# Optimization experiments

Hardware: AMD Instinct MI355X
Metric: run time of the kernel (lower is better)

Reference implementation:

```python
import jax, jax.numpy as jnp
import numpy as np

B, S, D, H = 1, 2048, 1024, 16
DH = D // H  # 64
HID = 4 * D
EPS = 1e-5
NEG = -1.0e9


def setup_inputs() -> dict:
    key = jax.random.key(0)
    ks = jax.random.split(key, 12)
    s = 0.02
    return {
        "y": jax.random.normal(ks[0], (B, S, D), jnp.float32),
        "encoder_output": jax.random.normal(ks[1], (B, S, D), jnp.float32),
        # per-head shared projection (query_fc used for q,k,v — faithful to source bug)
        "Wq_self": jax.random.normal(ks[2], (H, D, DH), jnp.float32) * s,
        "bq_self": jax.random.normal(ks[3], (H, DH), jnp.float32) * s,
        "Wq_cross": jax.random.normal(ks[4], (H, D, DH), jnp.float32) * s,
        "bq_cross": jax.random.normal(ks[5], (H, DH), jnp.float32) * s,
        "g1": jnp.ones((D,), jnp.float32), "beta1": jnp.zeros((D,), jnp.float32),
        "g2": jnp.ones((D,), jnp.float32), "beta2": jnp.zeros((D,), jnp.float32),
        "g3": jnp.ones((D,), jnp.float32), "beta3": jnp.zeros((D,), jnp.float32),
        "w1": jax.random.normal(ks[6], (D, HID), jnp.float32) * s,
        "b1": jax.random.normal(ks[7], (HID,), jnp.float32) * s,
        "w2": jax.random.normal(ks[8], (HID, D), jnp.float32) * s,
        "b2": jax.random.normal(ks[9], (D,), jnp.float32) * s,
    }


def _layernorm(x, g, b):
    mu = jnp.mean(x, axis=-1, keepdims=True)
    var = jnp.mean((x - mu) ** 2, axis=-1, keepdims=True)
    return (x - mu) * jax.lax.rsqrt(var + EPS) * g + b


def _mha(x_q, x_kv, W, bias, causal):
    # source bug: q, k, v all use query_fc projection
    q = jnp.einsum('bsd,hde->bhse', x_q, W) + bias[None, :, None, :]
    k = jnp.einsum('bsd,hde->bhse', x_kv, W) + bias[None, :, None, :]
    v = jnp.einsum('bsd,hde->bhse', x_kv, W) + bias[None, :, None, :]
    scores = jnp.einsum('bhse,bhte->bhst', q, k) / jnp.sqrt(jnp.float32(DH))
    if causal:
        sq, sk = scores.shape[-2], scores.shape[-1]
        mask = jnp.triu(jnp.ones((sq, sk), bool), k=1)
        scores = jnp.where(mask, NEG, scores)
    p = jax.nn.softmax(scores, axis=-1)
    out = jnp.einsum('bhst,bhte->bhse', p, v)  # [B,H,S,DH]
    b, h, s, e = out.shape
    return out.transpose(0, 2, 1, 3).reshape(b, s, h * e)


def reference(y, encoder_output, Wq_self, bq_self, Wq_cross, bq_cross,
              g1, beta1, g2, beta2, g3, beta3, w1, b1, w2, b2):
    sa = _mha(y, y, Wq_self, bq_self, causal=True)
    y1 = _layernorm(y + sa, g1, beta1)
    ca = _mha(y1, encoder_output, Wq_cross, bq_cross, causal=False)
    y2 = _layernorm(y1 + ca, g2, beta2)
    ff = jnp.maximum(y2 @ w1 + b1, 0.0) @ w2 + b2
    return _layernorm(y2 + ff, g3, beta3)
```

## Files before the change

kernel.cpp:

```cpp
#include <hip/hip_runtime.h>
#include <hip/hip_bf16.h>


#define S_LEN 2048
#define DMODEL 1024
#define NHEAD 16
#define DHEAD 64
#define HIDDEN 4096

using bf16 = __hip_bfloat16;
typedef __attribute__((ext_vector_type(8))) short bf16x8;
typedef __attribute__((ext_vector_type(4))) float floatx4;

__device__ __forceinline__ void async_ld16(const void* g, void* l) {
  __builtin_amdgcn_global_load_lds(
      (const __attribute__((address_space(1))) unsigned int*)g,
      (__attribute__((address_space(3))) unsigned int*)l, 16, 0, 0);
}

__device__ __forceinline__ unsigned short f2bf_bits(float f) {
  __hip_bfloat16 b = __float2bfloat16(f);
  return *(unsigned short*)&b;
}

template <bool HEADB>
__global__ __launch_bounds__(256) void transp_bf16_kernel(
    const float* __restrict__ src0, bf16* __restrict__ dst0,
    const float* __restrict__ src1, bf16* __restrict__ dst1, int K, int N) {
  const float* src = blockIdx.z ? src1 : src0;
  bf16* dst = blockIdx.z ? dst1 : dst0;
  __shared__ float tile[32][33];
  const int tx = threadIdx.x & 31, ty = threadIdx.x >> 5;
  const int k0 = blockIdx.y * 32, n0 = blockIdx.x * 32;
#pragma unroll
  for (int i = 0; i < 4; ++i) {
    const int k = k0 + ty + i * 8;
    const int n = n0 + tx;
    size_t idx;
    if (HEADB)
      idx = (size_t)(n >> 6) * ((size_t)K * 64) + (size_t)k * 64 + (n & 63);
    else
      idx = (size_t)k * N + n;
    tile[ty + i * 8][tx] = src[idx];
  }
  __syncthreads();
#pragma unroll
  for (int i = 0; i < 4; ++i) {
    const int n = n0 + ty + i * 8;
    const int k = k0 + tx;
    dst[(size_t)n * K + k] = __float2bfloat16(tile[tx][ty + i * 8]);
  }
}

__global__ __launch_bounds__(256) void conv_bf16_kernel(
    const float* __restrict__ src0, bf16* __restrict__ dst0,
    const float* __restrict__ src1, bf16* __restrict__ dst1, int n4) {
  const float* src = blockIdx.z ? src1 : src0;
  bf16* dst = blockIdx.z ? dst1 : dst0;
  const int i = blockIdx.x * 256 + threadIdx.x;
  if (i >= n4) return;
  float4 v = ((const float4*)src)[i];
  unsigned short r[4] = {f2bf_bits(v.x), f2bf_bits(v.y), f2bf_bits(v.z), f2bf_bits(v.w)};
  ((ushort2*)dst)[i * 2] = make_ushort2(r[0], r[1]);
  ((ushort2*)dst)[i * 2 + 1] = make_ushort2(r[2], r[3]);
}

template <int BM, int BN, bool RELU, bool DUALT, typename CT>
__global__ __launch_bounds__(256) void mfma_gemm_kernel(
    const bf16* __restrict__ A0, const bf16* __restrict__ Bt0,
    const float* __restrict__ bias0, CT* __restrict__ C0,
    bf16* __restrict__ Ct0,
    const bf16* __restrict__ A1, const bf16* __restrict__ Bt1,
    const float* __restrict__ bias1, CT* __restrict__ C1,
    bf16* __restrict__ Ct1,
    int M, int N, int Kstride, int Klen) {
  const bf16* A = blockIdx.z ? A1 : A0;
  const bf16* Bt = blockIdx.z ? Bt1 : Bt0;
  const float* bias = blockIdx.z ? bias1 : bias0;
  CT* C = blockIdx.z ? C1 : C0;
  bf16* Ct = blockIdx.z ? Ct1 : Ct0;

  constexpr int MF = BM / 32;
  constexpr int NF = BN / 32;
  __shared__ __align__(16) bf16 As[BM * 64];
  __shared__ __align__(16) bf16 Bs[BN * 64];

  const int tid = threadIdx.x;
  const int wave = tid >> 6;
  const int lane = tid & 63;
  const int m0 = blockIdx.y * BM;
  const int n0 = blockIdx.x * BN;
  const int wr = wave >> 1, wc = wave & 1;

  const int srow = tid >> 3;
  const int schunk = (tid & 7) ^ (srow & 7);
  const bf16* agp = A + (size_t)(m0 + srow) * Kstride + schunk * 8;
  const bf16* bgp = Bt + (size_t)(n0 + srow) * Kstride + schunk * 8;
  char* alds = (char*)As + wave * 1024;
  char* blds = (char*)Bs + wave * 1024;

  floatx4 acc[MF][NF];
#pragma unroll
  for (int i = 0; i < MF; ++i)
#pragma unroll
    for (int j = 0; j < NF; ++j) acc[i][j] = floatx4{0.f, 0.f, 0.f, 0.f};

  const int mrow = lane & 15;
  const int p0 = (((lane >> 4) ^ (mrow & 7)) << 4);
  const int p1 = p0 ^ 64;

  for (int kt = 0; kt < Klen; kt += 64) {
    __syncthreads();
#pragma unroll
    for (int i = 0; i < BM / 32; ++i)
      async_ld16(agp + (size_t)(32 * i) * Kstride + kt, alds + i * 4096);
#pragma unroll
    for (int i = 0; i < BN / 32; ++i)
      async_ld16(bgp + (size_t)(32 * i) * Kstride + kt, blds + i * 4096);
    __syncthreads();

    bf16x8 af0[MF], af1[MF], bf0[NF], bf1[NF];
#pragma unroll
    for (int fi = 0; fi < MF; ++fi) {
      const char* ar = (char*)As + (wr * (BM / 2) + fi * 16 + mrow) * 128;
      af0[fi] = *(const bf16x8*)(ar + p0);
      af1[fi] = *(const bf16x8*)(ar + p1);
    }
#pragma unroll
    for (int fj = 0; fj < NF; ++fj) {
      const char* br = (char*)Bs + (wc * (BN / 2) + fj * 16 + mrow) * 128;
      bf0[fj] = *(const bf16x8*)(br + p0);
      bf1[fj] = *(const bf16x8*)(br + p1);
    }
#pragma unroll
    for (int fi = 0; fi < MF; ++fi)
#pragma unroll
      for (int fj = 0; fj < NF; ++fj) {
        acc[fi][fj] = __builtin_amdgcn_mfma_f32_16x16x32_bf16(
            af0[fi], bf0[fj], acc[fi][fj], 0, 0, 0);
        acc[fi][fj] = __builtin_amdgcn_mfma_f32_16x16x32_bf16(
            af1[fi], bf1[fj], acc[fi][fj], 0, 0, 0);
      }
  }

  const int erow = (lane >> 4) * 4;
  const int ecol = lane & 15;
#pragma unroll
  for (int fi = 0; fi < MF; ++fi) {
#pragma unroll
    for (int fj = 0; fj < NF; ++fj) {
      const int nn = n0 + wc * (BN / 2) + fj * 16 + ecol;
      const float bv = bias ? bias[nn] : 0.0f;
      const int mmb = m0 + wr * (BM / 2) + fi * 16 + erow;
      float v[4];
#pragma unroll
      for (int r = 0; r < 4; ++r) {
        v[r] = acc[fi][fj][r] + bv;
        if (RELU) v[r] = fmaxf(v[r], 0.0f);
        if constexpr (sizeof(CT) == 2)
          C[(size_t)(mmb + r) * N + nn] = (CT)__float2bfloat16(v[r]);
        else
          C[(size_t)(mmb + r) * N + nn] = (CT)v[r];
      }
      if (DUALT) {
        ushort4 pk;
        pk.x = f2bf_bits(v[0]);
        pk.y = f2bf_bits(v[1]);
        pk.z = f2bf_bits(v[2]);
        pk.w = f2bf_bits(v[3]);
        *(ushort4*)&Ct[(size_t)nn * M + mmb] = pk;
      }
    }
  }
}

__global__ __launch_bounds__(128) void mfma_attn_kernel(
    const bf16* __restrict__ Q, const bf16* __restrict__ K,
    const bf16* __restrict__ Vt,
    float* __restrict__ OA, float* __restrict__ OB,
    float* __restrict__ LA, float* __restrict__ LB, int causal) {
  __shared__ __align__(16) unsigned short Kt[64 * 64];
  __shared__ __align__(16) unsigned short Vs[64 * 64];
  __shared__ unsigned short Ps[2][32][72];

  const int tid = threadIdx.x;
  const int w = tid >> 6, lane = tid & 63;
  const int g = lane >> 4, c = lane & 15;
  const int h = blockIdx.y;
  const int q0 = blockIdx.x * 64;
  const int z = blockIdx.z;
  const int qw = q0 + w * 32;
  float* Oz = z ? OB : OA;
  float* Lz = z ? LB : LA;

  bf16x8 qf0[2], qf1[2];
#pragma unroll
  for (int qs = 0; qs < 2; ++qs) {
    const bf16* qrow =
        Q + (size_t)(qw + qs * 16 + c) * DMODEL + h * DHEAD + g * 8;
    qf0[qs] = *(const bf16x8*)qrow;
    qf1[qs] = *(const bf16x8*)(qrow + 32);
  }

  const int srow = tid >> 3;
  const int schunk = (tid & 7) ^ (srow & 7);
  const bf16* kgp = K + (size_t)srow * DMODEL + h * DHEAD + schunk * 8;
  const bf16* vgp = Vt + (size_t)(h * DHEAD + srow) * S_LEN + schunk * 8;
  char* klds = (char*)Kt + w * 1024;
  char* vlds = (char*)Vs + w * 1024;

  const int kpos0 = ((g ^ (c & 7)) << 4);
  const int kpos1 = kpos0 ^ 64;

  floatx4 of[4][2];
#pragma unroll
  for (int md = 0; md < 4; ++md)
#pragma unroll
    for (int qs = 0; qs < 2; ++qs) of[md][qs] = floatx4{0.f, 0.f, 0.f, 0.f};
  float lpart[2] = {0.f, 0.f};

  const int nkt = causal ? (q0 / 64 + 1) : (S_LEN / 64);
  for (int kt = z; kt < nkt; kt += 2) {
    const int t0 = kt * 64;

    __syncthreads();
#pragma unroll
    for (int i = 0; i < 4; ++i) {
      async_ld16(kgp + (size_t)(t0 + 16 * i) * DMODEL, klds + i * 2048);
      async_ld16(vgp + (size_t)(16 * i) * S_LEN + t0, vlds + i * 2048);
    }
    __syncthreads();

    const bool diag = causal && (t0 == q0);
#pragma unroll
    for (int jt = 0; jt < 4; ++jt) {
      const char* kr = (const char*)Kt + (16 * jt + c) * 128;
      const bf16x8 kf0 = *(const bf16x8*)(kr + kpos0);
      const bf16x8 kf1 = *(const bf16x8*)(kr + kpos1);
#pragma unroll
      for (int qs = 0; qs < 2; ++qs) {
        floatx4 s = floatx4{0.f, 0.f, 0.f, 0.f};
        s = __builtin_amdgcn_mfma_f32_16x16x32_bf16(kf0, qf0[qs], s, 0, 0, 0);
        s = __builtin_amdgcn_mfma_f32_16x16x32_bf16(kf1, qf1[qs], s, 0, 0, 0);

        ushort4 pk;
        unsigned short* pp = (unsigned short*)&pk;
#pragma unroll
        for (int r = 0; r < 4; ++r) {
          float p = __expf(0.125f * s[r]);
          if (diag && (t0 + 16 * jt + 4 * g + r > qw + qs * 16 + c)) p = 0.0f;
          lpart[qs] += p;
          pp[r] = f2bf_bits(p);
        }
        *(ushort4*)&Ps[w][qs * 16 + c][16 * jt + 4 * g] = pk;
      }
    }

#pragma unroll
    for (int ks = 0; ks < 2; ++ks) {
      const bf16x8 pf0 = *(const bf16x8*)&Ps[w][c][32 * ks + 8 * g];
      const bf16x8 pf1 = *(const bf16x8*)&Ps[w][16 + c][32 * ks + 8 * g];
      const int vpos = ks ? kpos1 : kpos0;
#pragma unroll
      for (int md = 0; md < 4; ++md) {
        const bf16x8 vf =
            *(const bf16x8*)((const char*)Vs + (md * 16 + c) * 128 + vpos);
        of[md][0] = __builtin_amdgcn_mfma_f32_16x16x32_bf16(vf, pf0, of[md][0], 0, 0, 0);
        of[md][1] = __builtin_amdgcn_mfma_f32_16x16x32_bf16(vf, pf1, of[md][1], 0, 0, 0);
      }
    }
  }

#pragma unroll
  for (int qs = 0; qs < 2; ++qs) {
    lpart[qs] += __shfl_xor(lpart[qs], 16, 64);
    lpart[qs] += __shfl_xor(lpart[qs], 32, 64);
    if (g == 0) Lz[(size_t)h * S_LEN + qw + qs * 16 + c] = lpart[qs];
    float* orow = Oz + (size_t)(qw + qs * 16 + c) * DMODEL + h * DHEAD;
#pragma unroll
    for (int md = 0; md < 4; ++md) {
      float4 v;
      v.x = of[md][qs][0];
      v.y = of[md][qs][1];
      v.z = of[md][qs][2];
      v.w = of[md][qs][3];
      *(float4*)(orow + md * 16 + 4 * g) = v;
    }
  }
}

template <bool DUAL, bool MERGE, bool SUM2>
__global__ __launch_bounds__(256) void add_ln_kernel(
    const float* __restrict__ X, const float* __restrict__ R,
    const float* __restrict__ R2, const float* __restrict__ bvec,
    const float* __restrict__ La, const float* __restrict__ Lb,
    const float* __restrict__ g, const float* __restrict__ beta,
    float* __restrict__ out, bf16* __restrict__ out2) {
  const int row = blockIdx.x;
  const int tid = threadIdx.x;

  float v[4];
  float s1 = 0.0f, s2 = 0.0f;
#pragma unroll
  for (int i = 0; i < 4; ++i) {
    const int c = tid + i * 256;
    float x = X[(size_t)row * DMODEL + c];
    if (MERGE) {
      const int h = c >> 6;
      const float rl =
          1.0f / (La[(size_t)h * S_LEN + row] + Lb[(size_t)h * S_LEN + row]);
      x += (R[(size_t)row * DMODEL + c] + R2[(size_t)row * DMODEL + c]) * rl;
    } else if (SUM2) {
      x += R[(size_t)row * DMODEL + c] + R2[(size_t)row * DMODEL + c] + bvec[c];
    } else {
      x += R[(size_t)row * DMODEL + c];
    }
    v[i] = x;
    s1 += x;
    s2 += x * x;
  }
#pragma unroll
  for (int off = 32; off; off >>= 1) {
    s1 += __shfl_xor(s1, off, 64);
    s2 += __shfl_xor(s2, off, 64);
  }
  __shared__ float w1s[4], w2s[4];
  const int wid = tid >> 6, lane = tid & 63;
  if (lane == 0) { w1s[wid] = s1; w2s[wid] = s2; }
  __syncthreads();
  s1 = w1s[0] + w1s[1] + w1s[2] + w1s[3];
  s2 = w2s[0] + w2s[1] + w2s[2] + w2s[3];

  const float mu = s1 * (1.0f / DMODEL);
  const float var = s2 * (1.0f / DMODEL) - mu * mu;
  const float rstd = rsqrtf(var + 1e-5f);

#pragma unroll
  for (int i = 0; i < 4; ++i) {
    const int c = tid + i * 256;
    const float r = (v[i] - mu) * rstd * g[c] + beta[c];
    out[(size_t)row * DMODEL + c] = r;
    if (DUAL) out2[(size_t)row * DMODEL + c] = __float2bfloat16(r);
  }
}

extern "C" void kernel_launch(void* const* d_in, const int* in_sizes, int n_in,
                              void* d_out, int out_size, void* d_ws, size_t ws_size,
                              hipStream_t stream) {
  const float* y      = (const float*)d_in[0];
  const float* enc    = (const float*)d_in[1];
  const float* Wself  = (const float*)d_in[2];
  const float* bself  = (const float*)d_in[3];
  const float* Wcross = (const float*)d_in[4];
  const float* bcross = (const float*)d_in[5];
  const float* g1     = (const float*)d_in[6];
  const float* be1    = (const float*)d_in[7];
  const float* g2     = (const float*)d_in[8];
  const float* be2    = (const float*)d_in[9];
  const float* g3     = (const float*)d_in[10];
  const float* be3    = (const float*)d_in[11];
  const float* w1     = (const float*)d_in[12];
  const float* b1     = (const float*)d_in[13];
  const float* w2     = (const float*)d_in[14];
  const float* b2     = (const float*)d_in[15];
  float* out = (float*)d_out;

  char* ws = (char*)d_ws;
  const size_t MB = 1024 * 1024;
  bf16*  ybf   = (bf16*)(ws + 0 * MB);
  bf16*  encbf = (bf16*)(ws + 4 * MB);
  float* PA    = (float*)(ws + 0 * MB);
  float* PB    = (float*)(ws + 8 * MB);
  float* Y1    = (float*)(ws + 16 * MB);
  float* Y2    = (float*)(ws + 24 * MB);
  bf16*  Q12b  = (bf16*)(ws + 32 * MB);
  bf16*  Q1t   = (bf16*)(ws + 36 * MB);
  bf16*  K2b   = (bf16*)(ws + 40 * MB);
  bf16*  K2t   = (bf16*)(ws + 44 * MB);
  bf16*  w1t   = (bf16*)(ws + 48 * MB);
  bf16*  w2t   = (bf16*)(ws + 56 * MB);
  bf16*  Wst   = (bf16*)(ws + 64 * MB);
  bf16*  Wct   = (bf16*)(ws + 66 * MB);
  bf16*  Y1bf  = (bf16*)(ws + 68 * MB);
  bf16*  Y2bf  = (bf16*)(ws + 72 * MB);
  float* La    = (float*)(ws + 76 * MB);
  float* Lb    = (float*)(ws + 76 * MB + 512 * 1024);
  bf16*  FFH   = (bf16*)(ws + 0 * MB);
  float* FFa   = (float*)(ws + 32 * MB);
  float* FFb   = (float*)(ws + 40 * MB);

  const dim3 blk(256);
  const dim3 blkA(128);
  const dim3 gT_w(DMODEL / 32, DMODEL / 32, 2);
  const dim3 gT_w1(HIDDEN / 32, DMODEL / 32);
  const dim3 gT_w2(DMODEL / 32, HIDDEN / 32);
  const dim3 gConv(S_LEN * DMODEL / 4 / 256, 1, 2);
  const dim3 gProj2(DMODEL / 64, S_LEN / 64, 2);
  const dim3 gProj(DMODEL / 64, S_LEN / 64);
  const dim3 gFf1(HIDDEN / 128, S_LEN / 64);
  const dim3 gFf2(DMODEL / 64, S_LEN / 64, 2);
  const dim3 gAttn(S_LEN / 64, NHEAD, 2);
  const dim3 gLn(S_LEN);

  transp_bf16_kernel<true><<<gT_w, blk, 0, stream>>>(
      Wself, Wst, Wcross, Wct, DMODEL, DMODEL);
  transp_bf16_kernel<false><<<gT_w1, blk, 0, stream>>>(
      w1, w1t, nullptr, nullptr, DMODEL, HIDDEN);
  transp_bf16_kernel<false><<<gT_w2, blk, 0, stream>>>(
      w2, w2t, nullptr, nullptr, HIDDEN, DMODEL);
  conv_bf16_kernel<<<gConv, blk, 0, stream>>>(
      y, ybf, enc, encbf, S_LEN * DMODEL / 4);

  mfma_gemm_kernel<64, 64, false, true, bf16><<<gProj2, blk, 0, stream>>>(
      ybf, Wst, bself, Q12b, Q1t,
      encbf, Wct, bcross, K2b, K2t, S_LEN, DMODEL, DMODEL, DMODEL);
  mfma_attn_kernel<<<gAttn, blkA, 0, stream>>>(
      Q12b, Q12b, Q1t, PA, PB, La, Lb, 1);
  add_ln_kernel<true, true, false><<<gLn, blk, 0, stream>>>(
      y, PA, PB, nullptr, La, Lb, g1, be1, Y1, Y1bf);
  mfma_gemm_kernel<64, 64, false, false, bf16><<<gProj, blk, 0, stream>>>(
      Y1bf, Wct, bcross, Q12b, nullptr,
      nullptr, nullptr, nullptr, nullptr, nullptr, S_LEN, DMODEL, DMODEL, DMODEL);
  mfma_attn_kernel<<<gAttn, blkA, 0, stream>>>(
      Q12b, K2b, K2t, PA, PB, La, Lb, 0);
  add_ln_kernel<true, true, false><<<gLn, blk, 0, stream>>>(
      Y1, PA, PB, nullptr, La, Lb, g2, be2, Y2, Y2bf);
  mfma_gemm_kernel<64, 128, true, false, bf16><<<gFf1, blk, 0, stream>>>(
      Y2bf, w1t, b1, FFH, nullptr,
      nullptr, nullptr, nullptr, nullptr, nullptr, S_LEN, HIDDEN, DMODEL, DMODEL);
  mfma_gemm_kernel<64, 64, false, false, float><<<gFf2, blk, 0, stream>>>(
      FFH, w2t, nullptr, FFa, nullptr,
      FFH + HIDDEN / 2, w2t + HIDDEN / 2, nullptr, FFb, nullptr,
      S_LEN, DMODEL, HIDDEN, HIDDEN / 2);
  add_ln_kernel<false, false, true><<<gLn, blk, 0, stream>>>(
      Y2, FFa, FFb, b2, nullptr, nullptr, g3, be3, out, nullptr);
}
```

Measured before the change: 314.3 us.

## Double-buffer LDS tiles in GEMM and attention, swizzle P, reverse causal blocks

The GEMM and attention kernels now use two LDS buffers. The next K tile is loaded asynchronously into one buffer while MFMA runs on the other, and each iteration ends with a single barrier instead of two. This hides global-load latency, at the cost of twice the LDS and possibly lower occupancy. The attention kernel also XOR-swizzles the P scratch layout to avoid bank conflicts, issues causal query blocks heaviest-first to balance load, and raises wave priority around the MFMA calls.

```diff
diff --git a/kernel.cpp b/kernel.cpp
--- a/kernel.cpp
+++ b/kernel.cpp
@@ -82,8 +82,8 @@
 
   constexpr int MF = BM / 32;
   constexpr int NF = BN / 32;
-  __shared__ __align__(16) bf16 As[BM * 64];
-  __shared__ __align__(16) bf16 Bs[BN * 64];
+  __shared__ __align__(16) bf16 As[2][BM * 64];
+  __shared__ __align__(16) bf16 Bs[2][BN * 64];
 
   const int tid = threadIdx.x;
   const int wave = tid >> 6;
@@ -96,8 +96,6 @@
   const int schunk = (tid & 7) ^ (srow & 7);
   const bf16* agp = A + (size_t)(m0 + srow) * Kstride + schunk * 8;
   const bf16* bgp = Bt + (size_t)(n0 + srow) * Kstride + schunk * 8;
-  char* alds = (char*)As + wave * 1024;
-  char* blds = (char*)Bs + wave * 1024;
 
   floatx4 acc[MF][NF];
 #pragma unroll
@@ -109,26 +107,36 @@
   const int p0 = (((lane >> 4) ^ (mrow & 7)) << 4);
   const int p1 = p0 ^ 64;
 
+  auto stage = [&](int buf, int kt) {
+    char* al = (char*)As + buf * (BM * 128) + wave * 1024;
+    char* bl = (char*)Bs + buf * (BN * 128) + wave * 1024;
+#pragma unroll
+    for (int i = 0; i < BM / 32; ++i)
+      async_ld16(agp + (size_t)(32 * i) * Kstride + kt, al + i * 4096);
+#pragma unroll
+    for (int i = 0; i < BN / 32; ++i)
+      async_ld16(bgp + (size_t)(32 * i) * Kstride + kt, bl + i * 4096);
+  };
+
+  stage(0, 0);
+  __syncthreads();
+
+  int cur = 0;
   for (int kt = 0; kt < Klen; kt += 64) {
-    __syncthreads();
-#pragma unroll
-    for (int i = 0; i < BM / 32; ++i)
-      async_ld16(agp + (size_t)(32 * i) * Kstride + kt, alds + i * 4096);
-#pragma unroll
-    for (int i = 0; i < BN / 32; ++i)
-      async_ld16(bgp + (size_t)(32 * i) * Kstride + kt, blds + i * 4096);
-    __syncthreads();
-
+    if (kt + 64 < Klen) stage(cur ^ 1, kt + 64);
+
+    const char* abase = (const char*)As + cur * (BM * 128);
+    const char* bbase = (const char*)Bs + cur * (BN * 128);
     bf16x8 af0[MF], af1[MF], bf0[NF], bf1[NF];
 #pragma unroll
     for (int fi = 0; fi < MF; ++fi) {
-      const char* ar = (char*)As + (wr * (BM / 2) + fi * 16 + mrow) * 128;
+      const char* ar = abase + (wr * (BM / 2) + fi * 16 + mrow) * 128;
       af0[fi] = *(const bf16x8*)(ar + p0);
       af1[fi] = *(const bf16x8*)(ar + p1);
     }
 #pragma unroll
     for (int fj = 0; fj < NF; ++fj) {
-      const char* br = (char*)Bs + (wc * (BN / 2) + fj * 16 + mrow) * 128;
+      const char* br = bbase + (wc * (BN / 2) + fj * 16 + mrow) * 128;
       bf0[fj] = *(const bf16x8*)(br + p0);
       bf1[fj] = *(const bf16x8*)(br + p1);
     }
@@ -141,6 +149,9 @@
         acc[fi][fj] = __builtin_amdgcn_mfma_f32_16x16x32_bf16(
             af1[fi], bf1[fj], acc[fi][fj], 0, 0, 0);
       }
+
+    __syncthreads();
+    cur ^= 1;
   }
 
   const int erow = (lane >> 4) * 4;
@@ -179,15 +190,17 @@
     const bf16* __restrict__ Vt,
     float* __restrict__ OA, float* __restrict__ OB,
     float* __restrict__ LA, float* __restrict__ LB, int causal) {
-  __shared__ __align__(16) unsigned short Kt[64 * 64];
-  __shared__ __align__(16) unsigned short Vs[64 * 64];
-  __shared__ unsigned short Ps[2][32][72];
+  __shared__ __align__(16) unsigned short Kt[2][64 * 64];
+  __shared__ __align__(16) unsigned short Vs[2][64 * 64];
+  __shared__ __align__(16) unsigned short Ps[2][2048];
 
   const int tid = threadIdx.x;
   const int w = tid >> 6, lane = tid & 63;
   const int g = lane >> 4, c = lane & 15;
   const int h = blockIdx.y;
-  const int q0 = blockIdx.x * 64;
+  const int qb = causal ? ((int)gridDim.x - 1 - (int)blockIdx.x)
+                        : (int)blockIdx.x;
+  const int q0 = qb * 64;
   const int z = blockIdx.z;
   const int qw = q0 + w * 32;
   float* Oz = z ? OB : OA;
@@ -206,8 +219,6 @@
   const int schunk = (tid & 7) ^ (srow & 7);
   const bf16* kgp = K + (size_t)srow * DMODEL + h * DHEAD + schunk * 8;
   const bf16* vgp = Vt + (size_t)(h * DHEAD + srow) * S_LEN + schunk * 8;
-  char* klds = (char*)Kt + w * 1024;
-  char* vlds = (char*)Vs + w * 1024;
 
   const int kpos0 = ((g ^ (c & 7)) << 4);
   const int kpos1 = kpos0 ^ 64;
@@ -220,28 +231,42 @@
   float lpart[2] = {0.f, 0.f};
 
   const int nkt = causal ? (q0 / 64 + 1) : (S_LEN / 64);
-  for (int kt = z; kt < nkt; kt += 2) {
+
+  auto stage = [&](int buf, int kt) {
     const int t0 = kt * 64;
-
-    __syncthreads();
+    char* klds = (char*)Kt + buf * 8192 + w * 1024;
+    char* vlds = (char*)Vs + buf * 8192 + w * 1024;
 #pragma unroll
     for (int i = 0; i < 4; ++i) {
       async_ld16(kgp + (size_t)(t0 + 16 * i) * DMODEL, klds + i * 2048);
       async_ld16(vgp + (size_t)(16 * i) * S_LEN + t0, vlds + i * 2048);
     }
-    __syncthreads();
+  };
+
+  if (z < nkt) stage(0, z);
+  __syncthreads();
+
+  int cur = 0;
+  for (int kt = z; kt < nkt; kt += 2) {
+    const int t0 = kt * 64;
+    if (kt + 2 < nkt) stage(cur ^ 1, kt + 2);
+
+    const char* kbase = (const char*)Kt + cur * 8192;
+    const char* vbase = (const char*)Vs + cur * 8192;
 
     const bool diag = causal && (t0 == q0);
 #pragma unroll
     for (int jt = 0; jt < 4; ++jt) {
-      const char* kr = (const char*)Kt + (16 * jt + c) * 128;
+      const char* kr = kbase + (16 * jt + c) * 128;
       const bf16x8 kf0 = *(const bf16x8*)(kr + kpos0);
       const bf16x8 kf1 = *(const bf16x8*)(kr + kpos1);
 #pragma unroll
       for (int qs = 0; qs < 2; ++qs) {
         floatx4 s = floatx4{0.f, 0.f, 0.f, 0.f};
+        __builtin_amdgcn_s_setprio(1);
         s = __builtin_amdgcn_mfma_f32_16x16x32_bf16(kf0, qf0[qs], s, 0, 0, 0);
         s = __builtin_amdgcn_mfma_f32_16x16x32_bf16(kf1, qf1[qs], s, 0, 0, 0);
+        __builtin_amdgcn_s_setprio(0);
 
         ushort4 pk;
         unsigned short* pp = (unsigned short*)&pk;
@@ -252,23 +277,31 @@
           lpart[qs] += p;
           pp[r] = f2bf_bits(p);
         }
-        *(ushort4*)&Ps[w][qs * 16 + c][16 * jt + 4 * g] = pk;
+        const int qq = qs * 16 + c;
+        const int pb = qq * 128 + ((8 * (4 * jt + g)) ^ ((qq & 7) << 4));
+        *(ushort4*)((char*)Ps[w] + pb) = pk;
       }
     }
 
 #pragma unroll
     for (int ks = 0; ks < 2; ++ks) {
-      const bf16x8 pf0 = *(const bf16x8*)&Ps[w][c][32 * ks + 8 * g];
-      const bf16x8 pf1 = *(const bf16x8*)&Ps[w][16 + c][32 * ks + 8 * g];
+      const int px = (64 * ks + 16 * g) ^ ((c & 7) << 4);
+      const bf16x8 pf0 = *(const bf16x8*)((const char*)Ps[w] + c * 128 + px);
+      const bf16x8 pf1 =
+          *(const bf16x8*)((const char*)Ps[w] + (16 + c) * 128 + px);
       const int vpos = ks ? kpos1 : kpos0;
 #pragma unroll
       for (int md = 0; md < 4; ++md) {
-        const bf16x8 vf =
-            *(const bf16x8*)((const char*)Vs + (md * 16 + c) * 128 + vpos);
+        const bf16x8 vf = *(const bf16x8*)(vbase + (md * 16 + c) * 128 + vpos);
+        __builtin_amdgcn_s_setprio(1);
         of[md][0] = __builtin_amdgcn_mfma_f32_16x16x32_bf16(vf, pf0, of[md][0], 0, 0, 0);
         of[md][1] = __builtin_amdgcn_mfma_f32_16x16x32_bf16(vf, pf1, of[md][1], 0, 0, 0);
+        __builtin_amdgcn_s_setprio(0);
       }
     }
+
+    __syncthreads();
+    cur ^= 1;
   }
 
 #pragma unroll
```

After: 313.8 us. About the same (-0.2%).
